# Performance work log

Hardware: AMD Instinct MI355X
Metric: run time of the kernel (lower is better)

## Reference

```python
import jax, jax.numpy as jnp
import numpy as np

N_NODES = 50000
N_EDGES = 500000
IN_CH = 128
HID = 32
HEADS = 4
OUT_CH = 64
NEG_SLOPE = 0.2


def setup_inputs() -> dict:
    key = jax.random.key(0)
    ks = jax.random.split(key, 12)
    s = 0.1  # weight init scale
    x = jax.random.normal(ks[0], (N_NODES, IN_CH), jnp.float32)
    edge_index = jax.random.randint(ks[1], (2, N_EDGES), 0, N_NODES)
    # conv1: GATv2Conv(IN_CH, HID, heads=HEADS)
    W1l = jax.random.normal(ks[2], (IN_CH, HEADS * HID), jnp.float32) * s  # lin_l (source)
    W1r = jax.random.normal(ks[3], (IN_CH, HEADS * HID), jnp.float32) * s  # lin_r (target)
    att1 = jax.random.normal(ks[4], (HEADS, HID), jnp.float32) * s
    b1 = jnp.zeros((HEADS * HID,), jnp.float32)
    # conv2: GATv2Conv(HEADS*HID, OUT_CH, heads=1, concat=False)
    W2l = jax.random.normal(ks[5], (HEADS * HID, OUT_CH), jnp.float32) * s
    W2r = jax.random.normal(ks[6], (HEADS * HID, OUT_CH), jnp.float32) * s
    att2 = jax.random.normal(ks[7], (1, OUT_CH), jnp.float32) * s
    b2 = jnp.zeros((OUT_CH,), jnp.float32)
    return {"x": x, "edge_index": edge_index, "W1l": W1l, "W1r": W1r,
            "att1": att1, "b1": b1, "W2l": W2l, "W2r": W2r, "att2": att2, "b2": b2}


def gatv2_conv(x, src, dst, Wl, Wr, att, heads, ch, num_nodes):
    """GATv2Conv message passing. Returns [N, heads, ch] (pre-bias, pre-concat)."""
    xl = (x @ Wl).reshape(num_nodes, heads, ch)  # source transform
    xr = (x @ Wr).reshape(num_nodes, heads, ch)  # target transform
    xl_e = xl[src]                               # [E, H, C] gathered source feats
    m = jax.nn.leaky_relu(xl_e + xr[dst], NEG_SLOPE)
    score = jnp.einsum('ehc,hc->eh', m, att)     # [E, H]
    # segment softmax over incoming edges per destination node
    smax = jax.ops.segment_max(score, dst, num_segments=num_nodes)
    smax = jnp.where(jnp.isfinite(smax), smax, 0.0)
    p = jnp.exp(score - smax[dst])
    denom = jax.ops.segment_sum(p, dst, num_segments=num_nodes)
    alpha = p / (denom[dst] + 1e-16)
    out = jax.ops.segment_sum(alpha[:, :, None] * xl_e, dst, num_segments=num_nodes)
    return out


def reference(x, edge_index, W1l, W1r, att1, b1, W2l, W2r, att2, b2):
    n = x.shape[0]
    loop = jnp.arange(n, dtype=edge_index.dtype)
    src = jnp.concatenate([edge_index[0], loop])  # add self-loops (PyG default)
    dst = jnp.concatenate([edge_index[1], loop])
    # dropout(p=0.6) is identity in eval mode
    h = gatv2_conv(x, src, dst, W1l, W1r, att1, HEADS, HID, n)
    h = h.reshape(n, HEADS * HID) + b1            # concat=True
    h = jax.nn.elu(h)
    o = gatv2_conv(h, src, dst, W2l, W2r, att2, 1, OUT_CH, n)  # [N, 1, OUT]
    o = o + b2                                     # concat=False, heads=1 -> mean == identity
    return o[:, 0, :]
```

## Files before the change

### kernel.cpp

```cpp
#include <hip/hip_runtime.h>
#include <hip/hip_bf16.h>
#include <math.h>

#define N_NODESC 50000
#define N_EDGESC 500000
#define E_TOT    (N_EDGESC + N_NODESC)
#define IN_CH 128
#define HID 32
#define HEADS 4
#define HC (HEADS*HID)
#define OUT_CH 64
#define NEG_SLOPE 0.2f
#define NB_SCAN 196
#define N_STRIPS (N_NODESC/16)

typedef unsigned short u16;
typedef __attribute__((ext_vector_type(8))) short short8;
typedef __attribute__((ext_vector_type(8))) unsigned short ushort8v;
typedef __attribute__((ext_vector_type(4))) unsigned short ushort4v;
typedef __attribute__((ext_vector_type(4))) float floatx4;

__device__ __forceinline__ u16 f2bf(float f){
  unsigned u = __float_as_uint(f);
  return (u16)((u + 0x7FFFu + ((u >> 16) & 1u)) >> 16);
}
__device__ __forceinline__ float bf2f(u16 b){ return __uint_as_float(((unsigned)b) << 16); }
__device__ __forceinline__ float lrelu(float v){ return (v > 0.f) ? v : NEG_SLOPE*v; }

__device__ __forceinline__ void edge_sd(const int* __restrict__ ei, int e, int& s, int& d){
  if (e < N_EDGESC){ s = ei[e]; d = ei[N_EDGESC + e]; }
  else { s = e - N_EDGESC; d = s; }
}

__global__ void k_zero_deg(int* __restrict__ deg){
  int i = blockIdx.x*blockDim.x + threadIdx.x;
  if (i < N_NODESC) deg[i] = 0;
}

__global__ void k_hist(const int* __restrict__ ei, int* __restrict__ deg){
  int e = blockIdx.x*blockDim.x + threadIdx.x;
  if (e >= E_TOT) return;
  int s, d; edge_sd(ei, e, s, d);
  atomicAdd(&deg[d], 1);
}

__global__ void k_scan_a(const int* __restrict__ deg, int* __restrict__ rs,
                         int* __restrict__ bsum){
  __shared__ int sh[256];
  int i = blockIdx.x*256 + threadIdx.x;
  int v = (i < N_NODESC) ? deg[i] : 0;
  sh[threadIdx.x] = v;
  __syncthreads();
  for (int off=1; off<256; off<<=1){
    int t = (threadIdx.x >= off) ? sh[threadIdx.x-off] : 0;
    __syncthreads();
    sh[threadIdx.x] += t;
    __syncthreads();
  }
  if (i < N_NODESC) rs[i] = sh[threadIdx.x] - v;
  if (threadIdx.x == 255) bsum[blockIdx.x] = sh[255];
}

__global__ void k_scan_b(int* __restrict__ bsum){
  __shared__ int sh[256];
  int v = (threadIdx.x < NB_SCAN) ? bsum[threadIdx.x] : 0;
  sh[threadIdx.x] = v;
  __syncthreads();
  for (int off=1; off<256; off<<=1){
    int t = (threadIdx.x >= off) ? sh[threadIdx.x-off] : 0;
    __syncthreads();
    sh[threadIdx.x] += t;
    __syncthreads();
  }
  if (threadIdx.x < NB_SCAN) bsum[threadIdx.x] = sh[threadIdx.x] - v;
}

__global__ void k_scan_c(int* __restrict__ rs, const int* __restrict__ bsum,
                         int* __restrict__ cursor){
  int i = blockIdx.x*256 + threadIdx.x;
  if (i >= N_NODESC) return;
  int v = rs[i] + bsum[blockIdx.x];
  rs[i] = v;
  cursor[i] = v;
}

__global__ void k_fill(const int* __restrict__ ei, int* __restrict__ cursor,
                       int* __restrict__ csrc){
  int e = blockIdx.x*blockDim.x + threadIdx.x;
  if (e >= E_TOT) return;
  int s, d; edge_sd(ei, e, s, d);
  int pos = atomicAdd(&cursor[d], 1);
  csrc[pos] = s;
}

__global__ void k_split(const float* __restrict__ X, u16* __restrict__ hi,
                        u16* __restrict__ lo, int total4){
  int i = blockIdx.x*blockDim.x + threadIdx.x;
  if (i >= total4) return;
  float4 v = ((const float4*)X)[i];
  ushort4 h, l;
  h.x = f2bf(v.x); l.x = f2bf(v.x - bf2f(h.x));
  h.y = f2bf(v.y); l.y = f2bf(v.y - bf2f(h.y));
  h.z = f2bf(v.z); l.z = f2bf(v.z - bf2f(h.z));
  h.w = f2bf(v.w); l.w = f2bf(v.w - bf2f(h.w));
  ((ushort4*)hi)[i] = h;
  ((ushort4*)lo)[i] = l;
}

__global__ void k_prep_all(const float* __restrict__ W1l, const float* __restrict__ W1r,
                           const float* __restrict__ W2l, const float* __restrict__ W2r,
                           u16* __restrict__ w1lh, u16* __restrict__ w1rh,
                           u16* __restrict__ w2lh, u16* __restrict__ w2rh){
  int b = blockIdx.x;
  const float* W; u16 *Th; int N, base;
  if (b < 8)      { W=W1l; Th=w1lh; N=HC;     base=b;    }
  else if (b < 16){ W=W1r; Th=w1rh; N=HC;     base=b-8;  }
  else if (b < 20){ W=W2l; Th=w2lh; N=OUT_CH; base=b-16; }
  else            { W=W2r; Th=w2rh; N=OUT_CH; base=b-20; }
  int tid = base*256 + threadIdx.x;
  int lane = tid & 63;
  int t = (tid >> 6) & 3;
  int c = tid >> 8;
  int k0 = t*32 + (lane>>4)*8;
  int n  = c*16 + (lane&15);
  #pragma unroll
  for (int j=0;j<8;j++){
    Th[(size_t)tid*8 + j] = f2bf(W[(size_t)(k0+j)*N + n]);
  }
}

template<int NCW, int SPB>
__launch_bounds__(256, 2)
__global__ void k_gemm_regB(const u16* __restrict__ Ahi, const u16* __restrict__ Alo,
                            const u16* __restrict__ BlT, const u16* __restrict__ BrT,
                            u16* __restrict__ Olb, float* __restrict__ Or){
  constexpr int NLD = 2*NCW*16;
  int wave = threadIdx.x >> 6, lane = threadIdx.x & 63;
  int m = lane & 15, quad = lane >> 4;
  bool isl = (wave < 2);
  int ctbase = (isl ? wave : wave - 2) * NCW;
  const u16* __restrict__ BT = isl ? BlT : BrT;

  short8 breg[NCW][4];
  #pragma unroll
  for (int c=0;c<NCW;c++)
    #pragma unroll
    for (int t=0;t<4;t++)
      breg[c][t] = *(const short8*)(BT + ((size_t)(((ctbase+c)*4 + t)*64) + lane)*8);

  int strip0 = blockIdx.x * SPB;
  short8 ah[2][4], al[2][4];

  {
    const u16* p1 = Ahi + (size_t)(strip0*16 + m)*128 + quad*8;
    const u16* p2 = Alo + (size_t)(strip0*16 + m)*128 + quad*8;
    #pragma unroll
    for (int t=0;t<4;t++){
      ah[0][t] = *(const short8*)(p1 + t*32);
      al[0][t] = *(const short8*)(p2 + t*32);
    }
  }

  #pragma unroll
  for (int i=0;i<SPB;i++){
    int s = strip0 + i;
    if (s >= N_STRIPS) break;
    if (i+1 < SPB && s+1 < N_STRIPS){
      const u16* p1 = Ahi + (size_t)((s+1)*16 + m)*128 + quad*8;
      const u16* p2 = Alo + (size_t)((s+1)*16 + m)*128 + quad*8;
      #pragma unroll
      for (int t=0;t<4;t++){
        ah[(i+1)&1][t] = *(const short8*)(p1 + t*32);
        al[(i+1)&1][t] = *(const short8*)(p2 + t*32);
      }
    }
    const int b = i&1;
    floatx4 acc[NCW];
    #pragma unroll
    for (int c=0;c<NCW;c++) acc[c] = (floatx4){0.f,0.f,0.f,0.f};
    #pragma unroll
    for (int t=0;t<4;t++){
      #pragma unroll
      for (int c=0;c<NCW;c++){
        acc[c] = __builtin_amdgcn_mfma_f32_16x16x32_bf16(ah[b][t], breg[c][t], acc[c], 0,0,0);
        acc[c] = __builtin_amdgcn_mfma_f32_16x16x32_bf16(al[b][t], breg[c][t], acc[c], 0,0,0);
      }
    }
    int row0 = s*16;
    if (isl){
      #pragma unroll
      for (int c=0;c<NCW;c++)
        #pragma unroll
        for (int r=0;r<4;r++)
          Olb[(size_t)(row0 + quad*4 + r)*NLD + (ctbase+c)*16 + m] = f2bf(acc[c][r]);
    } else {
      #pragma unroll
      for (int c=0;c<NCW;c++)
        #pragma unroll
        for (int r=0;r<4;r++)
          Or[(size_t)(row0 + quad*4 + r)*NLD + (ctbase+c)*16 + m] = acc[c][r];
    }
  }
}

__global__ void k_fused1(const int* __restrict__ rs, const int* __restrict__ deg,
                         const int* __restrict__ csrc, const u16* __restrict__ xlb,
                         const float* __restrict__ xr, const float* __restrict__ att,
                         const float* __restrict__ b1,
                         u16* __restrict__ Hhi, u16* __restrict__ Hlo){
  int wave = threadIdx.x >> 6;
  int lane = threadIdx.x & 63;
  int d = blockIdx.x*4 + wave;
  if (d >= N_NODESC) return;
  int g = lane >> 4;
  int l = lane & 15;

  float xrv[8], atv[8], bv[8];
  const float* xrp = xr + (size_t)d*HC + 8*l;
  #pragma unroll
  for (int j=0;j<8;j++){ xrv[j] = xrp[j]; atv[j] = att[8*l+j]; bv[j] = b1[8*l+j]; }

  int start = rs[d], degd = deg[d];

  float acc[8];
  #pragma unroll
  for (int j=0;j<8;j++) acc[j] = 0.f;
  float den = 0.f;

  int e0 = g;
  int s_cur = csrc[start + ((e0 < degd) ? e0 : 0)];
  for (int i = 0; i < degd; i += 4){
    bool valid = (i + g < degd);
    int s = s_cur;
    int en = i + 4 + g;
    s_cur = csrc[start + ((en < degd) ? en : 0)];
    ushort8v q = *(const ushort8v*)(xlb + (size_t)s*HC + 8*l);
    float xv[8];
    float sc = 0.f;
    #pragma unroll
    for (int j=0;j<8;j++){
      xv[j] = bf2f(q[j]);
      sc += lrelu(xv[j] + xrv[j]) * atv[j];
    }
    sc += __shfl_xor(sc, 1);
    sc += __shfl_xor(sc, 2);
    float p = valid ? __expf(sc) : 0.f;
    den += p;
    #pragma unroll
    for (int j=0;j<8;j++) acc[j] += p * xv[j];
  }
  #pragma unroll
  for (int j=0;j<8;j++){
    acc[j] += __shfl_xor(acc[j], 16);
    acc[j] += __shfl_xor(acc[j], 32);
  }
  den += __shfl_xor(den, 16);
  den += __shfl_xor(den, 32);

  if (g == 0){
    float inv = 1.f / (den + 1e-16f);
    ushort8v oh, ol;
    #pragma unroll
    for (int j=0;j<8;j++){
      float o = acc[j]*inv + bv[j];
      o = (o > 0.f) ? o : (__expf(o) - 1.f);
      u16 h = f2bf(o);
      oh[j] = h;
      ol[j] = f2bf(o - bf2f(h));
    }
    *(ushort8v*)(Hhi + (size_t)d*HC + 8*l) = oh;
    *(ushort8v*)(Hlo + (size_t)d*HC + 8*l) = ol;
  }
}

__global__ void k_fused2(const int* __restrict__ rs, const int* __restrict__ deg,
                         const int* __restrict__ csrc, const u16* __restrict__ xlb,
                         const float* __restrict__ xr, const float* __restrict__ att,
                         const float* __restrict__ b2, float* __restrict__ out){
  int wave = threadIdx.x >> 6;
  int lane = threadIdx.x & 63;
  int d = blockIdx.x*4 + wave;
  if (d >= N_NODESC) return;
  int g = lane >> 4;
  int l = lane & 15;

  float xrv[4], atv[4], bv[4];
  const float* xrp = xr + (size_t)d*OUT_CH + 4*l;
  #pragma unroll
  for (int j=0;j<4;j++){ xrv[j] = xrp[j]; atv[j] = att[4*l+j]; bv[j] = b2[4*l+j]; }

  int start = rs[d], degd = deg[d];

  float acc[4] = {0.f,0.f,0.f,0.f};
  float den = 0.f;

  int e0 = g;
  int s_cur = csrc[start + ((e0 < degd) ? e0 : 0)];
  for (int i = 0; i < degd; i += 4){
    bool valid = (i + g < degd);
    int s = s_cur;
    int en = i + 4 + g;
    s_cur = csrc[start + ((en < degd) ? en : 0)];
    ushort4v q = *(const ushort4v*)(xlb + (size_t)s*OUT_CH + 4*l);
    float xv[4];
    float sc = 0.f;
    #pragma unroll
    for (int j=0;j<4;j++){
      xv[j] = bf2f(q[j]);
      sc += lrelu(xv[j] + xrv[j]) * atv[j];
    }
    sc += __shfl_xor(sc, 1);
    sc += __shfl_xor(sc, 2);
    sc += __shfl_xor(sc, 4);
    sc += __shfl_xor(sc, 8);
    float p = valid ? __expf(sc) : 0.f;
    den += p;
    #pragma unroll
    for (int j=0;j<4;j++) acc[j] += p * xv[j];
  }
  #pragma unroll
  for (int j=0;j<4;j++){
    acc[j] += __shfl_xor(acc[j], 16);
    acc[j] += __shfl_xor(acc[j], 32);
  }
  den += __shfl_xor(den, 16);
  den += __shfl_xor(den, 32);

  if (g == 0){
    float inv = 1.f / (den + 1e-16f);
    float4 o;
    o.x = acc[0]*inv + bv[0];
    o.y = acc[1]*inv + bv[1];
    o.z = acc[2]*inv + bv[2];
    o.w = acc[3]*inv + bv[3];
    *(float4*)(out + (size_t)d*OUT_CH + 4*l) = o;
  }
}

extern "C" void kernel_launch(void* const* d_in, const int* in_sizes, int n_in,
                              void* d_out, int out_size, void* d_ws, size_t ws_size,
                              hipStream_t stream) {
  const float* x    = (const float*)d_in[0];
  const int*   ei   = (const int*)d_in[1];
  const float* W1l  = (const float*)d_in[2];
  const float* W1r  = (const float*)d_in[3];
  const float* att1 = (const float*)d_in[4];
  const float* b1   = (const float*)d_in[5];
  const float* W2l  = (const float*)d_in[6];
  const float* W2r  = (const float*)d_in[7];
  const float* att2 = (const float*)d_in[8];
  const float* b2   = (const float*)d_in[9];
  float* out = (float*)d_out;

  float* ws = (float*)d_ws;
  size_t off = 0;
  float* xr1 = ws + off; off += (size_t)N_NODESC*HC;
  float* xr2 = ws + off; off += (size_t)N_NODESC*OUT_CH;
  u16* xl1b = (u16*)(ws + off); off += (size_t)N_NODESC*HC/2;
  u16* xl2b = (u16*)(ws + off); off += (size_t)N_NODESC*OUT_CH/2;
  u16* xhi = (u16*)(ws + off); off += (size_t)N_NODESC*HC/2;
  u16* xlo = (u16*)(ws + off); off += (size_t)N_NODESC*HC/2;
  u16* hhi = (u16*)(ws + off); off += (size_t)N_NODESC*HC/2;
  u16* hlo = (u16*)(ws + off); off += (size_t)N_NODESC*HC/2;
  u16* w1lh = (u16*)(ws + off); off += IN_CH*HC/2;
  u16* w1rh = (u16*)(ws + off); off += IN_CH*HC/2;
  u16* w2lh = (u16*)(ws + off); off += HC*OUT_CH/2;
  u16* w2rh = (u16*)(ws + off); off += HC*OUT_CH/2;
  int* deg    = (int*)(ws + off); off += N_NODESC;
  int* rs     = (int*)(ws + off); off += N_NODESC;
  int* cursor = (int*)(ws + off); off += N_NODESC;
  int* bsum   = (int*)(ws + off); off += 256;
  int* csrc   = (int*)(ws + off); off += E_TOT;

  k_zero_deg<<<(N_NODESC+255)/256, 256, 0, stream>>>(deg);
  k_hist<<<(E_TOT+255)/256, 256, 0, stream>>>(ei, deg);
  k_scan_a<<<NB_SCAN, 256, 0, stream>>>(deg, rs, bsum);
  k_scan_b<<<1, 256, 0, stream>>>(bsum);
  k_scan_c<<<NB_SCAN, 256, 0, stream>>>(rs, bsum, cursor);
  k_fill<<<(E_TOT+255)/256, 256, 0, stream>>>(ei, cursor, csrc);

  k_split<<<((N_NODESC*HC/4)+255)/256, 256, 0, stream>>>(x, xhi, xlo, N_NODESC*HC/4);
  k_prep_all<<<24, 256, 0, stream>>>(W1l, W1r, W2l, W2r, w1lh, w1rh, w2lh, w2rh);

  const int NB_G = (N_STRIPS + 3)/4;
  k_gemm_regB<4,4><<<NB_G, 256, 0, stream>>>(xhi, xlo, w1lh, w1rh, xl1b, xr1);
  k_fused1<<<(N_NODESC+3)/4, 256, 0, stream>>>(rs, deg, csrc, xl1b, xr1, att1, b1, hhi, hlo);

  k_gemm_regB<2,4><<<NB_G, 256, 0, stream>>>(hhi, hlo, w2lh, w2rh, xl2b, xr2);
  k_fused2<<<(N_NODESC+3)/4, 256, 0, stream>>>(rs, deg, csrc, xl2b, xr2, att2, b2, out);
}
```

Baseline: 262.7 us.

## Store target projections in bf16, merge prep kernels, split fused1 launch

Merges the degree zeroing, weight conversion and x hi/lo split into one launch, and stores the target-side projections xr1/xr2 as bf16 instead of fp32, which halves their write and read traffic. It also uses explicit fma, a fmax-based leaky relu, and vectorised att and bias loads. It loads the bias only in the lanes that write output, and splits the first aggregation kernel into two half-size launches. Rounding xr to bf16 lowers precision in the attention scores, and the extra launch adds overhead.

```diff
diff --git a/kernel.cpp b/kernel.cpp
--- a/kernel.cpp
+++ b/kernel.cpp
@@ -25,16 +25,55 @@
   return (u16)((u + 0x7FFFu + ((u >> 16) & 1u)) >> 16);
 }
 __device__ __forceinline__ float bf2f(u16 b){ return __uint_as_float(((unsigned)b) << 16); }
-__device__ __forceinline__ float lrelu(float v){ return (v > 0.f) ? v : NEG_SLOPE*v; }
+__device__ __forceinline__ float bflo(unsigned q){ return __uint_as_float(q << 16); }
+__device__ __forceinline__ float bfhi(unsigned q){ return __uint_as_float(q & 0xFFFF0000u); }
+__device__ __forceinline__ float lrelu(float v){ return fmaxf(v, NEG_SLOPE*v); }
 
 __device__ __forceinline__ void edge_sd(const int* __restrict__ ei, int e, int& s, int& d){
   if (e < N_EDGESC){ s = ei[e]; d = ei[N_EDGESC + e]; }
   else { s = e - N_EDGESC; d = s; }
 }
 
-__global__ void k_zero_deg(int* __restrict__ deg){
-  int i = blockIdx.x*blockDim.x + threadIdx.x;
-  if (i < N_NODESC) deg[i] = 0;
+__global__ void k_misc(int* __restrict__ deg,
+                       const float* __restrict__ X, u16* __restrict__ xhi, u16* __restrict__ xlo,
+                       const float* __restrict__ W1l, const float* __restrict__ W1r,
+                       const float* __restrict__ W2l, const float* __restrict__ W2r,
+                       u16* __restrict__ w1lh, u16* __restrict__ w1rh,
+                       u16* __restrict__ w2lh, u16* __restrict__ w2rh){
+  int b = blockIdx.x;
+  if (b < 196){
+    int i = b*256 + threadIdx.x;
+    if (i < N_NODESC) deg[i] = 0;
+  } else if (b < 220){
+    int bb = b - 196;
+    const float* W; u16 *Th; int N, base;
+    if (bb < 8)      { W=W1l; Th=w1lh; N=HC;     base=bb;    }
+    else if (bb < 16){ W=W1r; Th=w1rh; N=HC;     base=bb-8;  }
+    else if (bb < 20){ W=W2l; Th=w2lh; N=OUT_CH; base=bb-16; }
+    else             { W=W2r; Th=w2rh; N=OUT_CH; base=bb-20; }
+    int tid = base*256 + threadIdx.x;
+    int lane = tid & 63;
+    int t = (tid >> 6) & 3;
+    int c = tid >> 8;
+    int k0 = t*32 + (lane>>4)*8;
+    int n  = c*16 + (lane&15);
+    #pragma unroll
+    for (int j=0;j<8;j++){
+      Th[(size_t)tid*8 + j] = f2bf(W[(size_t)(k0+j)*N + n]);
+    }
+  } else {
+    int i = (b-220)*256 + threadIdx.x;
+    if (i < N_NODESC*HC/4){
+      float4 v = ((const float4*)X)[i];
+      ushort4 h, l;
+      h.x = f2bf(v.x); l.x = f2bf(v.x - bf2f(h.x));
+      h.y = f2bf(v.y); l.y = f2bf(v.y - bf2f(h.y));
+      h.z = f2bf(v.z); l.z = f2bf(v.z - bf2f(h.z));
+      h.w = f2bf(v.w); l.w = f2bf(v.w - bf2f(h.w));
+      ((ushort4*)xhi)[i] = h;
+      ((ushort4*)xlo)[i] = l;
+    }
+  }
 }
 
 __global__ void k_hist(const int* __restrict__ ei, int* __restrict__ deg){
@@ -93,53 +132,18 @@
   csrc[pos] = s;
 }
 
-__global__ void k_split(const float* __restrict__ X, u16* __restrict__ hi,
-                        u16* __restrict__ lo, int total4){
-  int i = blockIdx.x*blockDim.x + threadIdx.x;
-  if (i >= total4) return;
-  float4 v = ((const float4*)X)[i];
-  ushort4 h, l;
-  h.x = f2bf(v.x); l.x = f2bf(v.x - bf2f(h.x));
-  h.y = f2bf(v.y); l.y = f2bf(v.y - bf2f(h.y));
-  h.z = f2bf(v.z); l.z = f2bf(v.z - bf2f(h.z));
-  h.w = f2bf(v.w); l.w = f2bf(v.w - bf2f(h.w));
-  ((ushort4*)hi)[i] = h;
-  ((ushort4*)lo)[i] = l;
-}
-
-__global__ void k_prep_all(const float* __restrict__ W1l, const float* __restrict__ W1r,
-                           const float* __restrict__ W2l, const float* __restrict__ W2r,
-                           u16* __restrict__ w1lh, u16* __restrict__ w1rh,
-                           u16* __restrict__ w2lh, u16* __restrict__ w2rh){
-  int b = blockIdx.x;
-  const float* W; u16 *Th; int N, base;
-  if (b < 8)      { W=W1l; Th=w1lh; N=HC;     base=b;    }
-  else if (b < 16){ W=W1r; Th=w1rh; N=HC;     base=b-8;  }
-  else if (b < 20){ W=W2l; Th=w2lh; N=OUT_CH; base=b-16; }
-  else            { W=W2r; Th=w2rh; N=OUT_CH; base=b-20; }
-  int tid = base*256 + threadIdx.x;
-  int lane = tid & 63;
-  int t = (tid >> 6) & 3;
-  int c = tid >> 8;
-  int k0 = t*32 + (lane>>4)*8;
-  int n  = c*16 + (lane&15);
-  #pragma unroll
-  for (int j=0;j<8;j++){
-    Th[(size_t)tid*8 + j] = f2bf(W[(size_t)(k0+j)*N + n]);
-  }
-}
-
 template<int NCW, int SPB>
 __launch_bounds__(256, 2)
 __global__ void k_gemm_regB(const u16* __restrict__ Ahi, const u16* __restrict__ Alo,
                             const u16* __restrict__ BlT, const u16* __restrict__ BrT,
-                            u16* __restrict__ Olb, float* __restrict__ Or){
+                            u16* __restrict__ Olb, u16* __restrict__ Orb){
   constexpr int NLD = 2*NCW*16;
   int wave = threadIdx.x >> 6, lane = threadIdx.x & 63;
   int m = lane & 15, quad = lane >> 4;
   bool isl = (wave < 2);
   int ctbase = (isl ? wave : wave - 2) * NCW;
   const u16* __restrict__ BT = isl ? BlT : BrT;
+  u16* __restrict__ Ob = isl ? Olb : Orb;
 
   short8 breg[NCW][4];
   #pragma unroll
@@ -187,38 +191,36 @@
       }
     }
     int row0 = s*16;
-    if (isl){
+    #pragma unroll
+    for (int c=0;c<NCW;c++)
       #pragma unroll
-      for (int c=0;c<NCW;c++)
-        #pragma unroll
-        for (int r=0;r<4;r++)
-          Olb[(size_t)(row0 + quad*4 + r)*NLD + (ctbase+c)*16 + m] = f2bf(acc[c][r]);
-    } else {
-      #pragma unroll
-      for (int c=0;c<NCW;c++)
-        #pragma unroll
-        for (int r=0;r<4;r++)
-          Or[(size_t)(row0 + quad*4 + r)*NLD + (ctbase+c)*16 + m] = acc[c][r];
-    }
+      for (int r=0;r<4;r++)
+        Ob[(size_t)(row0 + quad*4 + r)*NLD + (ctbase+c)*16 + m] = f2bf(acc[c][r]);
   }
 }
 
 __global__ void k_fused1(const int* __restrict__ rs, const int* __restrict__ deg,
                          const int* __restrict__ csrc, const u16* __restrict__ xlb,
-                         const float* __restrict__ xr, const float* __restrict__ att,
+                         const u16* __restrict__ xrb, const float* __restrict__ att,
                          const float* __restrict__ b1,
-                         u16* __restrict__ Hhi, u16* __restrict__ Hlo){
+                         u16* __restrict__ Hhi, u16* __restrict__ Hlo, int d0){
   int wave = threadIdx.x >> 6;
   int lane = threadIdx.x & 63;
-  int d = blockIdx.x*4 + wave;
+  int d = d0 + blockIdx.x*4 + wave;
   if (d >= N_NODESC) return;
   int g = lane >> 4;
   int l = lane & 15;
 
-  float xrv[8], atv[8], bv[8];
-  const float* xrp = xr + (size_t)d*HC + 8*l;
-  #pragma unroll
-  for (int j=0;j<8;j++){ xrv[j] = xrp[j]; atv[j] = att[8*l+j]; bv[j] = b1[8*l+j]; }
+  float xrv[8], atv[8];
+  {
+    ushort8v xq = *(const ushort8v*)(xrb + (size_t)d*HC + 8*l);
+    #pragma unroll
+    for (int j=0;j<8;j++) xrv[j] = bf2f(xq[j]);
+    float4 c = *(const float4*)(att + 8*l);
+    float4 e = *(const float4*)(att + 8*l + 4);
+    atv[0]=c.x; atv[1]=c.y; atv[2]=c.z; atv[3]=c.w;
+    atv[4]=e.x; atv[5]=e.y; atv[6]=e.z; atv[7]=e.w;
+  }
 
   int start = rs[d], degd = deg[d];
 
@@ -227,8 +229,7 @@
   for (int j=0;j<8;j++) acc[j] = 0.f;
   float den = 0.f;
 
-  int e0 = g;
-  int s_cur = csrc[start + ((e0 < degd) ? e0 : 0)];
+  int s_cur = csrc[start + ((g < degd) ? g : 0)];
   for (int i = 0; i < degd; i += 4){
     bool valid = (i + g < degd);
     int s = s_cur;
@@ -240,14 +241,14 @@
     #pragma unroll
     for (int j=0;j<8;j++){
       xv[j] = bf2f(q[j]);
-      sc += lrelu(xv[j] + xrv[j]) * atv[j];
+      sc = fmaf(lrelu(xv[j] + xrv[j]), atv[j], sc);
     }
     sc += __shfl_xor(sc, 1);
     sc += __shfl_xor(sc, 2);
     float p = valid ? __expf(sc) : 0.f;
     den += p;
     #pragma unroll
-    for (int j=0;j<8;j++) acc[j] += p * xv[j];
+    for (int j=0;j<8;j++) acc[j] = fmaf(p, xv[j], acc[j]);
   }
   #pragma unroll
   for (int j=0;j<8;j++){
@@ -258,24 +259,33 @@
   den += __shfl_xor(den, 32);
 
   if (g == 0){
+    float bv[8];
+    float4 a = *(const float4*)(b1 + 8*l);
+    float4 b = *(const float4*)(b1 + 8*l + 4);
+    bv[0]=a.x; bv[1]=a.y; bv[2]=a.z; bv[3]=a.w;
+    bv[4]=b.x; bv[5]=b.y; bv[6]=b.z; bv[7]=b.w;
     float inv = 1.f / (den + 1e-16f);
-    ushort8v oh, ol;
+    u16 ohv[8], olv[8];
     #pragma unroll
     for (int j=0;j<8;j++){
       float o = acc[j]*inv + bv[j];
       o = (o > 0.f) ? o : (__expf(o) - 1.f);
       u16 h = f2bf(o);
-      oh[j] = h;
-      ol[j] = f2bf(o - bf2f(h));
-    }
-    *(ushort8v*)(Hhi + (size_t)d*HC + 8*l) = oh;
-    *(ushort8v*)(Hlo + (size_t)d*HC + 8*l) = ol;
+      ohv[j] = h;
+      olv[j] = f2bf(o - bf2f(h));
+    }
+    ushort4 h0 = {ohv[0],ohv[1],ohv[2],ohv[3]}, h1 = {ohv[4],ohv[5],ohv[6],ohv[7]};
+    ushort4 l0 = {olv[0],olv[1],olv[2],olv[3]}, l1 = {olv[4],olv[5],olv[6],olv[7]};
+    *(ushort4*)(Hhi + (size_t)d*HC + 8*l)     = h0;
+    *(ushort4*)(Hhi + (size_t)d*HC + 8*l + 4) = h1;
+    *(ushort4*)(Hlo + (size_t)d*HC + 8*l)     = l0;
+    *(ushort4*)(Hlo + (size_t)d*HC + 8*l + 4) = l1;
   }
 }
 
 __global__ void k_fused2(const int* __restrict__ rs, const int* __restrict__ deg,
                          const int* __restrict__ csrc, const u16* __restrict__ xlb,
-                         const float* __restrict__ xr, const float* __restrict__ att,
+                         const u16* __restrict__ xrb, const float* __restrict__ att,
                          const float* __restrict__ b2, float* __restrict__ out){
   int wave = threadIdx.x >> 6;
   int lane = threadIdx.x & 63;
@@ -284,31 +294,33 @@
   int g = lane >> 4;
   int l = lane & 15;
 
-  float xrv[4], atv[4], bv[4];
-  const float* xrp = xr + (size_t)d*OUT_CH + 4*l;
-  #pragma unroll
-  for (int j=0;j<4;j++){ xrv[j] = xrp[j]; atv[j] = att[4*l+j]; bv[j] = b2[4*l+j]; }
+  float xrv[4], atv[4];
+  {
+    ushort4v xq = *(const ushort4v*)(xrb + (size_t)d*OUT_CH + 4*l);
+    #pragma unroll
+    for (int j=0;j<4;j++) xrv[j] = bf2f(xq[j]);
+    float4 c = *(const float4*)(att + 4*l);
+    atv[0]=c.x; atv[1]=c.y; atv[2]=c.z; atv[3]=c.w;
+  }
 
   int start = rs[d], degd = deg[d];
 
   float acc[4] = {0.f,0.f,0.f,0.f};
   float den = 0.f;
 
-  int e0 = g;
-  int s_cur = csrc[start + ((e0 < degd) ? e0 : 0)];
+  int s_cur = csrc[start + ((g < degd) ? g : 0)];
   for (int i = 0; i < degd; i += 4){
     bool valid = (i + g < degd);
     int s = s_cur;
     int en = i + 4 + g;
     s_cur = csrc[start + ((en < degd) ? en : 0)];
-    ushort4v q = *(const ushort4v*)(xlb + (size_t)s*OUT_CH + 4*l);
+    uint2 q = *(const uint2*)(xlb + (size_t)s*OUT_CH + 4*l);
     float xv[4];
+    xv[0]=bflo(q.x); xv[1]=bfhi(q.x);
+    xv[2]=bflo(q.y); xv[3]=bfhi(q.y);
     float sc = 0.f;
     #pragma unroll
-    for (int j=0;j<4;j++){
-      xv[j] = bf2f(q[j]);
-      sc += lrelu(xv[j] + xrv[j]) * atv[j];
-    }
+    for (int j=0;j<4;j++) sc = fmaf(lrelu(xv[j] + xrv[j]), atv[j], sc);
     sc += __shfl_xor(sc, 1);
     sc += __shfl_xor(sc, 2);
     sc += __shfl_xor(sc, 4);
@@ -316,7 +328,7 @@
     float p = valid ? __expf(sc) : 0.f;
     den += p;
     #pragma unroll
-    for (int j=0;j<4;j++) acc[j] += p * xv[j];
+    for (int j=0;j<4;j++) acc[j] = fmaf(p, xv[j], acc[j]);
   }
   #pragma unroll
   for (int j=0;j<4;j++){
@@ -327,12 +339,13 @@
   den += __shfl_xor(den, 32);
 
   if (g == 0){
+    float4 bvv = *(const float4*)(b2 + 4*l);
     float inv = 1.f / (den + 1e-16f);
     float4 o;
-    o.x = acc[0]*inv + bv[0];
-    o.y = acc[1]*inv + bv[1];
-    o.z = acc[2]*inv + bv[2];
-    o.w = acc[3]*inv + bv[3];
+    o.x = acc[0]*inv + bvv.x;
+    o.y = acc[1]*inv + bvv.y;
+    o.z = acc[2]*inv + bvv.z;
+    o.w = acc[3]*inv + bvv.w;
     *(float4*)(out + (size_t)d*OUT_CH + 4*l) = o;
   }
 }
@@ -354,10 +367,10 @@
 
   float* ws = (float*)d_ws;
   size_t off = 0;
-  float* xr1 = ws + off; off += (size_t)N_NODESC*HC;
-  float* xr2 = ws + off; off += (size_t)N_NODESC*OUT_CH;
   u16* xl1b = (u16*)(ws + off); off += (size_t)N_NODESC*HC/2;
+  u16* xr1b = (u16*)(ws + off); off += (size_t)N_NODESC*HC/2;
   u16* xl2b = (u16*)(ws + off); off += (size_t)N_NODESC*OUT_CH/2;
+  u16* xr2b = (u16*)(ws + off); off += (size_t)N_NODESC*OUT_CH/2;
   u16* xhi = (u16*)(ws + off); off += (size_t)N_NODESC*HC/2;
   u16* xlo = (u16*)(ws + off); off += (size_t)N_NODESC*HC/2;
   u16* hhi = (u16*)(ws + off); off += (size_t)N_NODESC*HC/2;
@@ -372,20 +385,19 @@
   int* bsum   = (int*)(ws + off); off += 256;
   int* csrc   = (int*)(ws + off); off += E_TOT;
 
-  k_zero_deg<<<(N_NODESC+255)/256, 256, 0, stream>>>(deg);
+  k_misc<<<220 + (N_NODESC*HC/4 + 255)/256, 256, 0, stream>>>(
+      deg, x, xhi, xlo, W1l, W1r, W2l, W2r, w1lh, w1rh, w2lh, w2rh);
   k_hist<<<(E_TOT+255)/256, 256, 0, stream>>>(ei, deg);
   k_scan_a<<<NB_SCAN, 256, 0, stream>>>(deg, rs, bsum);
   k_scan_b<<<1, 256, 0, stream>>>(bsum);
   k_scan_c<<<NB_SCAN, 256, 0, stream>>>(rs, bsum, cursor);
   k_fill<<<(E_TOT+255)/256, 256, 0, stream>>>(ei, cursor, csrc);
 
-  k_split<<<((N_NODESC*HC/4)+255)/256, 256, 0, stream>>>(x, xhi, xlo, N_NODESC*HC/4);
-  k_prep_all<<<24, 256, 0, stream>>>(W1l, W1r, W2l, W2r, w1lh, w1rh, w2lh, w2rh);
-
   const int NB_G = (N_STRIPS + 3)/4;
-  k_gemm_regB<4,4><<<NB_G, 256, 0, stream>>>(xhi, xlo, w1lh, w1rh, xl1b, xr1);
-  k_fused1<<<(N_NODESC+3)/4, 256, 0, stream>>>(rs, deg, csrc, xl1b, xr1, att1, b1, hhi, hlo);
-
-  k_gemm_regB<2,4><<<NB_G, 256, 0, stream>>>(hhi, hlo, w2lh, w2rh, xl2b, xr2);
-  k_fused2<<<(N_NODESC+3)/4, 256, 0, stream>>>(rs, deg, csrc, xl2b, xr2, att2, b2, out);
-}
+  k_gemm_regB<4,4><<<NB_G, 256, 0, stream>>>(xhi, xlo, w1lh, w1rh, xl1b, xr1b);
+  k_fused1<<<(N_NODESC/2+3)/4, 256, 0, stream>>>(rs, deg, csrc, xl1b, xr1b, att1, b1, hhi, hlo, 0);
+  k_fused1<<<(N_NODESC/2+3)/4, 256, 0, stream>>>(rs, deg, csrc, xl1b, xr1b, att1, b1, hhi, hlo, N_NODESC/2);
+
+  k_gemm_regB<2,4><<<NB_G, 256, 0, stream>>>(hhi, hlo, w2lh, w2rh, xl2b, xr2b);
+  k_fused2<<<(N_NODESC+3)/4, 256, 0, stream>>>(rs, deg, csrc, xl2b, xr2b, att2, b2, out);
+}
```

Result: no change. 264.9 us (+0.8%).
